# Kernel optimization log

Hardware: AMD Instinct MI355X
Metric: run time of the kernel (lower is better)

Reference implementation:

```python
import jax, jax.numpy as jnp
import numpy as np

E = 8  # moe_num_experts


def setup_inputs() -> dict:
    key = jax.random.key(0)
    ks = jax.random.split(key, 6)
    T, H, F, K = 8192, 768, 3072, 2
    x = jax.random.normal(ks[0], (T, H), dtype=jnp.float32)
    weights = jax.random.uniform(ks[1], (T, E), dtype=jnp.float32)
    top_weights = jax.random.uniform(ks[2], (T, K), dtype=jnp.float32)
    top_experts = jax.random.randint(ks[3], (T, K), 0, E)
    w1 = jax.random.normal(ks[4], (E, F, H), dtype=jnp.float32) * 0.02
    w2 = jax.random.normal(ks[5], (E, F, H), dtype=jnp.float32) * 0.02
    bias = jnp.zeros((H,), dtype=jnp.float32)
    return {"x": x, "weights": weights, "top_weights": top_weights,
            "top_experts": top_experts, "w1": w1, "w2": w2, "bias": bias}


def reference(x, weights, top_weights, top_experts, w1, w2, bias):
    # combine[t, e] = sum_k top_weights[t, k] * 1[top_experts[t, k] == e]
    one_hot = jax.nn.one_hot(top_experts, E, dtype=x.dtype)  # [T, K, E]
    combine = jnp.einsum('tke,tk->te', one_hot, top_weights)  # [T, E]
    out = jnp.zeros_like(x)
    for e in range(E):  # fixed small expert loop
        h = jax.nn.gelu(x @ w1[e].T, approximate=False)  # [T, F]
        out = out + (h @ w2[e]) * combine[:, e:e + 1]
    return out + bias
```

## Files before the change

kernel.cpp:

```cpp
#include <hip/hip_runtime.h>
#include <math.h>

#define TT   8192
#define HH   768
#define FF   3072
#define NEXP 8
#define NP   16384
#define BM   128
#define MAXT 135
#define MTP  136
#define ESTR (FF*HH)

typedef unsigned short u16;
typedef __attribute__((ext_vector_type(8))) short bf16x8;
typedef __attribute__((ext_vector_type(4))) float f32x4;

__device__ __forceinline__ u16 f2b(float f) {
  unsigned u = __float_as_uint(f);
  unsigned r = (u + 0x7FFFu + ((u >> 16) & 1u)) >> 16;
  return (u16)r;
}

__device__ __forceinline__ float gelu_exact(float v) {
  return 0.5f * v * (1.0f + erff(v * 0.70710678118654752f));
}

__device__ __forceinline__ void gll16(const void* g, void* l) {
  __builtin_amdgcn_global_load_lds(
      (const __attribute__((address_space(1))) void*)g,
      (__attribute__((address_space(3))) void*)l, 16, 0, 0);
}

__global__ __launch_bounds__(1024)
void route_all(const int* __restrict__ te, const float* __restrict__ tw,
               int* __restrict__ hdr) {
  __shared__ int cnt[NEXP], offs[NEXP], cur[NEXP];
  const int tid = threadIdx.x;
  const int lane = tid & 63, wave = tid >> 6;
  if (tid < NEXP) cnt[tid] = 0;
  __syncthreads();
  for (int base = wave * 64; base < NP; base += 1024) {
    int e = te[base + lane];
#pragma unroll
    for (int x = 0; x < NEXP; ++x) {
      unsigned long long m = __ballot(e == x);
      if (lane == 0 && m) atomicAdd(&cnt[x], __popcll(m));
    }
  }
  __syncthreads();
  if (tid == 0) {
    int run = 0, tt = 0;
#pragma unroll
    for (int x = 0; x < NEXP; ++x) {
      offs[x] = run; cur[x] = run;
      hdr[x] = cnt[x]; hdr[16 + x] = run;
      run += cnt[x];
    }
    for (int x = 0; x < NEXP; ++x) {
      int nt = (cnt[x] + BM - 1) >> 7;
      for (int i = 0; i < nt; ++i) { hdr[32 + tt] = x; hdr[192 + tt] = i * BM; ++tt; }
    }
    hdr[24] = tt;
  }
  __syncthreads();
  for (int base = wave * 64; base < NP; base += 1024) {
    int i = base + lane;
    int e = te[i];
    float w = tw[i];
    int slot = 0;
#pragma unroll
    for (int x = 0; x < NEXP; ++x) {
      unsigned long long m = __ballot(e == x);
      int nb = __popcll(m);
      int below = __popcll(m & ((1ull << lane) - 1ull));
      int b = 0;
      if (lane == 0) b = nb ? atomicAdd(&cur[x], nb) : 0;
      b = __shfl(b, 0);
      if (e == x) slot = b + below;
    }
    hdr[352 + slot] = i >> 1;
    ((float*)(hdr + 16736))[slot] = w;
    hdr[33120 + i] = slot;
  }
}

__global__ void cvt_all(const float* __restrict__ x, const float* __restrict__ w1,
                        u16* __restrict__ dst, int xn4, int totn4) {
  for (int i = blockIdx.x * 256 + threadIdx.x; i < totn4; i += gridDim.x * 256) {
    float4 v = (i < xn4) ? ((const float4*)x)[i] : ((const float4*)w1)[i - xn4];
    ushort4 o;
    o.x = f2b(v.x); o.y = f2b(v.y); o.z = f2b(v.z); o.w = f2b(v.w);
    ((ushort4*)dst)[i] = o;
  }
}

__global__ void transpose_w2(const float* __restrict__ w2, u16* __restrict__ w2t) {
  __shared__ u16 t[64][65];
  int e = blockIdx.z;
  int f0 = blockIdx.x * 64, h0 = blockIdx.y * 64;
  int tid = threadIdx.x;
  int tx = tid & 15, ty = tid >> 4;
  const float* s = w2 + (size_t)e * ESTR;
#pragma unroll
  for (int j = 0; j < 4; ++j) {
    int f = f0 + ty + 16 * j;
    float4 v = *(const float4*)&s[(size_t)f * HH + h0 + tx * 4];
    t[ty + 16 * j][tx * 4 + 0] = f2b(v.x);
    t[ty + 16 * j][tx * 4 + 1] = f2b(v.y);
    t[ty + 16 * j][tx * 4 + 2] = f2b(v.z);
    t[ty + 16 * j][tx * 4 + 3] = f2b(v.w);
  }
  __syncthreads();
  u16* d = w2t + (size_t)e * ESTR;
#pragma unroll
  for (int j = 0; j < 4; ++j) {
    int hr = ty + 16 * j;
    ushort4 o;
    o.x = t[tx * 4 + 0][hr];
    o.y = t[tx * 4 + 1][hr];
    o.z = t[tx * 4 + 2][hr];
    o.w = t[tx * 4 + 3][hr];
    *(ushort4*)&d[(size_t)(h0 + hr) * FF + f0 + tx * 4] = o;
  }
}

__global__ void bias_init(float* __restrict__ out, const float* __restrict__ bias) {
  int i = blockIdx.x * 256 + threadIdx.x;
  if (i < TT * HH / 4)
    ((float4*)out)[i] = ((const float4*)bias)[i % (HH / 4)];
}

__global__ void combine(const float* __restrict__ part, const int* __restrict__ hdr,
                        const float* __restrict__ bias, float* __restrict__ out) {
  int t = blockIdx.x;
  int c = threadIdx.x;
  const int* inv = hdr + 33120;
  const float* pw = (const float*)(hdr + 16736);
  int g0 = inv[2 * t], g1 = inv[2 * t + 1];
  float w0 = pw[g0], w1 = pw[g1];
  float4 p0 = ((const float4*)(part + (size_t)g0 * HH))[c];
  float4 p1 = ((const float4*)(part + (size_t)g1 * HH))[c];
  float4 b  = ((const float4*)bias)[c];
  float4 o;
  o.x = b.x + w0 * p0.x + w1 * p1.x;
  o.y = b.y + w0 * p0.y + w1 * p1.y;
  o.z = b.z + w0 * p0.z + w1 * p1.z;
  o.w = b.w + w0 * p0.w + w1 * p1.w;
  ((float4*)(out + (size_t)t * HH))[c] = o;
}

template <int PHASE, int NT, int G, int KS>
__global__ __launch_bounds__(256, 3)
void moe_gemm(const u16* __restrict__ Asrc, const u16* __restrict__ Bsrc,
              u16* __restrict__ Hout, float* __restrict__ Out,
              const int* __restrict__ hdr) {
  constexpr int KEXT = (PHASE == 1) ? HH : (FF / KS);
  constexpr int AST  = (PHASE == 1) ? HH : FF;
  constexpr int BST  = (PHASE == 1) ? HH : FF;
  constexpr int NK   = KEXT / 32;

  const int nwg = NT * MTP * KS;
  const int bid = blockIdx.x;
  const int l   = (bid & 7) * (nwg >> 3) + (bid >> 3);
  const int mtl = l % G;
  const int nt  = (l / G) % NT;
  const int kg  = (l / (G * NT)) % KS;
  const int sg  = l / (G * NT * KS);
  const int mt  = sg * G + mtl;
  if (mt >= hdr[24]) return;
  const int kbase = kg * KEXT;

  const int e   = hdr[32 + mt];
  const int m0  = hdr[192 + mt];
  const int cnt = hdr[e];
  const int off = hdr[16 + e];
  const int* ptok = hdr + 352;

  __shared__ u16 Al[3][4096];
  __shared__ u16 Bl[3][4096];

  const int tid  = threadIdx.x;
  const int lane = tid & 63;
  const int wave = tid >> 6;
  const int wm = wave >> 1, wn = wave & 1;
  const int lr = lane & 15;

  const int kcs = (((tid & 3) ^ ((tid >> 3) & 3)) * 8);
  const u16* aptr[2];
  const u16* bptr[2];
#pragma unroll
  for (int i = 0; i < 2; ++i) {
    int r = (tid >> 2) + 64 * i;
    if (PHASE == 1) {
      int g = off + m0 + r; g = g < NP ? g : NP - 1;
      aptr[i] = Asrc + (size_t)ptok[g] * AST + kcs;
    } else {
      int gr = off + m0 + r; gr = gr < NP ? gr : NP - 1;
      aptr[i] = Asrc + (size_t)gr * AST + kbase + kcs;
    }
    int br = nt * BM + r;
    bptr[i] = Bsrc + (size_t)e * ESTR + (size_t)br * BST + kbase + kcs;
  }

  f32x4 acc[4][4] = {};
  const int pcs = (((lane >> 4) ^ ((lane >> 1) & 3)) * 8);

#define STG(BS, T) do {                              \
    gll16(aptr[0] + (T) * 32, &Al[BS][tid * 8]);     \
    gll16(aptr[1] + (T) * 32, &Al[BS][tid * 8 + 2048]); \
    gll16(bptr[0] + (T) * 32, &Bl[BS][tid * 8]);     \
    gll16(bptr[1] + (T) * 32, &Bl[BS][tid * 8 + 2048]); \
  } while (0)

#define ITER(BC, BS, TSTG, DOST, VMN) do {                                   \
    asm volatile("s_waitcnt vmcnt(" #VMN ")" ::: "memory");                  \
    __builtin_amdgcn_sched_barrier(0);                                       \
    __builtin_amdgcn_s_barrier();                                            \
    bf16x8 af[4], bfr[4];                                                    \
    _Pragma("unroll")                                                        \
    for (int i = 0; i < 4; ++i)                                              \
      af[i] = *(const bf16x8*)&Al[BC][(wm * 64 + i * 16 + lr) * 32 + pcs];   \
    _Pragma("unroll")                                                        \
    for (int i = 0; i < 4; ++i)                                              \
      bfr[i] = *(const bf16x8*)&Bl[BC][(wn * 64 + i * 16 + lr) * 32 + pcs];  \
    if (DOST) STG(BS, TSTG);                                                 \
    asm volatile("s_waitcnt lgkmcnt(0)" ::: "memory");                       \
    __builtin_amdgcn_sched_barrier(0);                                       \
    __builtin_amdgcn_s_setprio(1);                                           \
    _Pragma("unroll")                                                        \
    for (int mi = 0; mi < 4; ++mi)                                           \
      _Pragma("unroll")                                                      \
      for (int ni = 0; ni < 4; ++ni)                                         \
        acc[mi][ni] = __builtin_amdgcn_mfma_f32_16x16x32_bf16(               \
            af[mi], bfr[ni], acc[mi][ni], 0, 0, 0);                          \
    __builtin_amdgcn_s_setprio(0);                                           \
  } while (0)

  STG(0, 0);
  STG(1, 1);

  for (int g = 0; g < NK / 3 - 1; ++g) {
    const int t0 = g * 3;
    ITER(0, 2, t0 + 2, 1, 4);
    ITER(1, 0, t0 + 3, 1, 4);
    ITER(2, 1, t0 + 4, 1, 4);
  }
  ITER(0, 2, NK - 1, 1, 4);
  ITER(1, 0, 0, 0, 4);
  ITER(2, 0, 0, 0, 0);
#undef ITER
#undef STG

  if (PHASE == 1) {
#pragma unroll
    for (int mi = 0; mi < 4; ++mi)
#pragma unroll
      for (int ni = 0; ni < 4; ++ni)
#pragma unroll
        for (int j = 0; j < 4; ++j) {
          int rl = wm * 64 + mi * 16 + (lane >> 4) * 4 + j;
          int gr = m0 + rl;
          if (gr < cnt) {
            int col = nt * BM + wn * 64 + ni * 16 + lr;
            Hout[(size_t)(off + gr) * FF + col] = f2b(gelu_exact(acc[mi][ni][j]));
          }
        }
  } else {
#pragma unroll
    for (int mi = 0; mi < 4; ++mi)
#pragma unroll
      for (int ni = 0; ni < 4; ++ni)
#pragma unroll
        for (int j = 0; j < 4; ++j) {
          int rl = wm * 64 + mi * 16 + (lane >> 4) * 4 + j;
          int gr = m0 + rl;
          if (gr < cnt) {
            int col = nt * BM + wn * 64 + ni * 16 + lr;
            Out[(size_t)(off + gr) * HH + col] = acc[mi][ni][j];
          }
        }
  }
}

__global__ void naive_pair(const float* __restrict__ x, const float* __restrict__ tw,
                           const int* __restrict__ te, const float* __restrict__ w1,
                           const float* __restrict__ w2, float* __restrict__ out) {
  __shared__ float xs[HH];
  __shared__ float hb[FF];
  int t = blockIdx.x >> 1, k = blockIdx.x & 1;
  int e = te[t * 2 + k];
  float wt = tw[t * 2 + k];
  for (int i = threadIdx.x; i < HH; i += 256) xs[i] = x[(size_t)t * HH + i];
  __syncthreads();
  const float* W1 = w1 + (size_t)e * ESTR;
  for (int f = threadIdx.x; f < FF; f += 256) {
    float s = 0.f;
    const float* r = W1 + (size_t)f * HH;
    for (int i = 0; i < HH; ++i) s += xs[i] * r[i];
    hb[f] = gelu_exact(s);
  }
  __syncthreads();
  const float* W2 = w2 + (size_t)e * ESTR;
  for (int c = threadIdx.x; c < HH; c += 256) {
    float s = 0.f;
    for (int f = 0; f < FF; ++f) s += hb[f] * W2[(size_t)f * HH + c];
    atomicAdd(&out[(size_t)t * HH + c], s * wt);
  }
}

extern "C" void kernel_launch(void* const* d_in, const int* in_sizes, int n_in,
                              void* d_out, int out_size, void* d_ws, size_t ws_size,
                              hipStream_t stream) {
  const float* x    = (const float*)d_in[0];
  const float* topw = (const float*)d_in[2];
  const int*   tope = (const int*)d_in[3];
  const float* w1   = (const float*)d_in[4];
  const float* w2   = (const float*)d_in[5];
  const float* bias = (const float*)d_in[6];
  float* out = (float*)d_out;

  char* ws = (char*)d_ws;
  const size_t HDRB   = 1u << 18;
  const size_t xb_off  = HDRB;
  const size_t xb_sz   = (size_t)TT * HH * 2;
  const size_t w1_off  = xb_off + xb_sz;
  const size_t w1_sz   = (size_t)NEXP * ESTR * 2;
  const size_t w2t_off = w1_off + w1_sz;
  const size_t w2t_sz  = w1_sz;
  const size_t h_off   = w2t_off + w2t_sz;
  const size_t h_sz    = (size_t)NP * FF * 2;
  const size_t need    = h_off + h_sz;

  if (ws_size < need) {
    bias_init<<<(TT * HH / 4 + 255) / 256, 256, 0, stream>>>(out, bias);
    naive_pair<<<NP, 256, 0, stream>>>(x, topw, tope, w1, w2, out);
    return;
  }

  int* hdr   = (int*)ws;
  u16* xb    = (u16*)(ws + xb_off);
  u16* w1b   = (u16*)(ws + w1_off);
  u16* w2t   = (u16*)(ws + w2t_off);
  u16* h     = (u16*)(ws + h_off);
  float* part = (float*)(ws + xb_off);

  route_all<<<1, 1024, 0, stream>>>(tope, topw, hdr);

  const int XN4 = TT * HH / 4;
  const int TOTN4 = (TT * HH + NEXP * ESTR) / 4;
  cvt_all<<<2048, 256, 0, stream>>>(x, w1, xb, XN4, TOTN4);
  transpose_w2<<<dim3(FF / 64, HH / 64, NEXP), 256, 0, stream>>>(w2, w2t);

  moe_gemm<1, 24, 8, 1><<<24 * MTP, 256, 0, stream>>>(xb, w1b, h, nullptr, hdr);
  moe_gemm<2, 6, 4, 1><<<6 * MTP, 256, 0, stream>>>(h, w2t, nullptr, part, hdr);
  combine<<<TT, HH / 4, 0, stream>>>(part, hdr, bias, out);
}
```

Before: 356.1 us.

## Load B operand directly to registers and deepen A LDS pipeline to four stages

The grouped MoE GEMM no longer stages the weight (B) tile through LDS. Each wave loads its B fragments straight from global memory into double-buffered registers, one k-step ahead. Only the gathered activation (A) tile still goes through LDS, now with a 4-deep ring buffer and a vmcnt(2) wait. Halving the LDS footprint lets launch_bounds rise to 4 blocks per CU, and the unused KS split-K template parameter is removed; the trade-off is uncoalesced per-lane B loads and more register pressure.

After: 720.9 us. +102.4%, slower.

```diff
diff --git a/kernel.cpp b/kernel.cpp
--- a/kernel.cpp
+++ b/kernel.cpp
@@ -34,7 +34,7 @@
 __global__ __launch_bounds__(1024)
 void route_all(const int* __restrict__ te, const float* __restrict__ tw,
                int* __restrict__ hdr) {
-  __shared__ int cnt[NEXP], offs[NEXP], cur[NEXP];
+  __shared__ int cnt[NEXP], cur[NEXP];
   const int tid = threadIdx.x;
   const int lane = tid & 63, wave = tid >> 6;
   if (tid < NEXP) cnt[tid] = 0;
@@ -52,7 +52,7 @@
     int run = 0, tt = 0;
 #pragma unroll
     for (int x = 0; x < NEXP; ++x) {
-      offs[x] = run; cur[x] = run;
+      cur[x] = run;
       hdr[x] = cnt[x]; hdr[16 + x] = run;
       run += cnt[x];
     }
@@ -149,26 +149,24 @@
   ((float4*)(out + (size_t)t * HH))[c] = o;
 }
 
-template <int PHASE, int NT, int G, int KS>
-__global__ __launch_bounds__(256, 3)
+template <int PHASE, int NT, int G>
+__global__ __launch_bounds__(256, 4)
 void moe_gemm(const u16* __restrict__ Asrc, const u16* __restrict__ Bsrc,
               u16* __restrict__ Hout, float* __restrict__ Out,
               const int* __restrict__ hdr) {
-  constexpr int KEXT = (PHASE == 1) ? HH : (FF / KS);
+  constexpr int KEXT = (PHASE == 1) ? HH : FF;
   constexpr int AST  = (PHASE == 1) ? HH : FF;
   constexpr int BST  = (PHASE == 1) ? HH : FF;
   constexpr int NK   = KEXT / 32;
 
-  const int nwg = NT * MTP * KS;
+  const int nwg = NT * MTP;
   const int bid = blockIdx.x;
   const int l   = (bid & 7) * (nwg >> 3) + (bid >> 3);
   const int mtl = l % G;
   const int nt  = (l / G) % NT;
-  const int kg  = (l / (G * NT)) % KS;
-  const int sg  = l / (G * NT * KS);
+  const int sg  = l / (G * NT);
   const int mt  = sg * G + mtl;
   if (mt >= hdr[24]) return;
-  const int kbase = kg * KEXT;
 
   const int e   = hdr[32 + mt];
   const int m0  = hdr[192 + mt];
@@ -176,8 +174,7 @@
   const int off = hdr[16 + e];
   const int* ptok = hdr + 352;
 
-  __shared__ u16 Al[3][4096];
-  __shared__ u16 Bl[3][4096];
+  __shared__ u16 Al[4][4096];
 
   const int tid  = threadIdx.x;
   const int lane = tid & 63;
@@ -187,7 +184,6 @@
 
   const int kcs = (((tid & 3) ^ ((tid >> 3) & 3)) * 8);
   const u16* aptr[2];
-  const u16* bptr[2];
 #pragma unroll
   for (int i = 0; i < 2; ++i) {
     int r = (tid >> 2) + 64 * i;
@@ -196,34 +192,43 @@
       aptr[i] = Asrc + (size_t)ptok[g] * AST + kcs;
     } else {
       int gr = off + m0 + r; gr = gr < NP ? gr : NP - 1;
-      aptr[i] = Asrc + (size_t)gr * AST + kbase + kcs;
-    }
-    int br = nt * BM + r;
-    bptr[i] = Bsrc + (size_t)e * ESTR + (size_t)br * BST + kbase + kcs;
+      aptr[i] = Asrc + (size_t)gr * AST + kcs;
+    }
+  }
+  const u16* bp[4];
+#pragma unroll
+  for (int q = 0; q < 4; ++q) {
+    int row = nt * BM + wn * 64 + q * 16 + lr;
+    bp[q] = Bsrc + (size_t)e * ESTR + (size_t)row * BST + (lane >> 4) * 8;
   }
 
   f32x4 acc[4][4] = {};
   const int pcs = (((lane >> 4) ^ ((lane >> 1) & 3)) * 8);
-
-#define STG(BS, T) do {                              \
-    gll16(aptr[0] + (T) * 32, &Al[BS][tid * 8]);     \
-    gll16(aptr[1] + (T) * 32, &Al[BS][tid * 8 + 2048]); \
-    gll16(bptr[0] + (T) * 32, &Bl[BS][tid * 8]);     \
-    gll16(bptr[1] + (T) * 32, &Bl[BS][tid * 8 + 2048]); \
+  bf16x8 brA[4], brB[4];
+
+#define STG(BS, T) do {                                   \
+    gll16(aptr[0] + (T) * 32, &Al[BS][tid * 8]);          \
+    gll16(aptr[1] + (T) * 32, &Al[BS][tid * 8 + 2048]);   \
   } while (0)
 
-#define ITER(BC, BS, TSTG, DOST, VMN) do {                                   \
+#define LDB(br, T) do {                                   \
+    _Pragma("unroll")                                     \
+    for (int q = 0; q < 4; ++q)                           \
+      br[q] = *(const bf16x8*)(bp[q] + (T) * 32);         \
+  } while (0)
+
+#define ITER(ABUF, brUSE, brLD, T, DOB, DOA, VMN) do {                       \
     asm volatile("s_waitcnt vmcnt(" #VMN ")" ::: "memory");                  \
     __builtin_amdgcn_sched_barrier(0);                                       \
     __builtin_amdgcn_s_barrier();                                            \
-    bf16x8 af[4], bfr[4];                                                    \
+    bf16x8 af[4];                                                            \
     _Pragma("unroll")                                                        \
     for (int i = 0; i < 4; ++i)                                              \
-      af[i] = *(const bf16x8*)&Al[BC][(wm * 64 + i * 16 + lr) * 32 + pcs];   \
-    _Pragma("unroll")                                                        \
-    for (int i = 0; i < 4; ++i)                                              \
-      bfr[i] = *(const bf16x8*)&Bl[BC][(wn * 64 + i * 16 + lr) * 32 + pcs];  \
-    if (DOST) STG(BS, TSTG);                                                 \
+      af[i] = *(const bf16x8*)&Al[ABUF][(wm * 64 + i * 16 + lr) * 32 + pcs]; \
+    if (DOB) LDB(brLD, (T) + 1);                                             \
+    __builtin_amdgcn_sched_barrier(0);                                       \
+    if (DOA) STG(((T) + 2) & 3, (T) + 2);                                    \
+    __builtin_amdgcn_sched_barrier(0);                                       \
     asm volatile("s_waitcnt lgkmcnt(0)" ::: "memory");                       \
     __builtin_amdgcn_sched_barrier(0);                                       \
     __builtin_amdgcn_s_setprio(1);                                           \
@@ -232,23 +237,27 @@
       _Pragma("unroll")                                                      \
       for (int ni = 0; ni < 4; ++ni)                                         \
         acc[mi][ni] = __builtin_amdgcn_mfma_f32_16x16x32_bf16(               \
-            af[mi], bfr[ni], acc[mi][ni], 0, 0, 0);                          \
+            af[mi], brUSE[ni], acc[mi][ni], 0, 0, 0);                        \
     __builtin_amdgcn_s_setprio(0);                                           \
   } while (0)
 
+  LDB(brA, 0);
+  __builtin_amdgcn_sched_barrier(0);
   STG(0, 0);
   STG(1, 1);
 
-  for (int g = 0; g < NK / 3 - 1; ++g) {
-    const int t0 = g * 3;
-    ITER(0, 2, t0 + 2, 1, 4);
-    ITER(1, 0, t0 + 3, 1, 4);
-    ITER(2, 1, t0 + 4, 1, 4);
-  }
-  ITER(0, 2, NK - 1, 1, 4);
-  ITER(1, 0, 0, 0, 4);
-  ITER(2, 0, 0, 0, 0);
+  for (int t0 = 0; t0 < NK - 4; t0 += 4) {
+    ITER(0, brA, brB, t0 + 0, 1, 1, 2);
+    ITER(1, brB, brA, t0 + 1, 1, 1, 2);
+    ITER(2, brA, brB, t0 + 2, 1, 1, 2);
+    ITER(3, brB, brA, t0 + 3, 1, 1, 2);
+  }
+  ITER(0, brA, brB, NK - 4, 1, 1, 2);
+  ITER(1, brB, brA, NK - 3, 1, 1, 2);
+  ITER(2, brA, brB, NK - 2, 1, 0, 2);
+  ITER(3, brB, brA, NK - 1, 0, 0, 0);
 #undef ITER
+#undef LDB
 #undef STG
 
   if (PHASE == 1) {
@@ -351,7 +360,7 @@
   cvt_all<<<2048, 256, 0, stream>>>(x, w1, xb, XN4, TOTN4);
   transpose_w2<<<dim3(FF / 64, HH / 64, NEXP), 256, 0, stream>>>(w2, w2t);
 
-  moe_gemm<1, 24, 8, 1><<<24 * MTP, 256, 0, stream>>>(xb, w1b, h, nullptr, hdr);
-  moe_gemm<2, 6, 4, 1><<<6 * MTP, 256, 0, stream>>>(h, w2t, nullptr, part, hdr);
+  moe_gemm<1, 24, 8><<<24 * MTP, 256, 0, stream>>>(xb, w1b, h, nullptr, hdr);
+  moe_gemm<2, 6, 4><<<6 * MTP, 256, 0, stream>>>(h, w2t, nullptr, part, hdr);
   combine<<<TT, HH / 4, 0, stream>>>(part, hdr, bias, out);
 }
```

## Use 256-row M tiles with 512-thread blocks for the first expert GEMM

Applied to the files above, without the earlier changes.

Splits the shared expert GEMM into two kernels. The first GEMM (x·w1 with GELU) now uses 256-row token tiles, 8 waves and 512 threads per block, so each loaded w1 tile feeds twice as many rows. This halves w1 reloads and the number of workgroups. The router builds a second tile list for the 256-row tiles in a new header region, and the second GEMM keeps its 128-row configuration. The cost is more padding waste in each expert's last tile, more LDS per block, and tighter register and occupancy limits from the 512-thread launch bounds.

Measured after the change: 350.7 us. Within noise of the previous version (-1.5%).

```diff
diff --git a/kernel.cpp b/kernel.cpp
--- a/kernel.cpp
+++ b/kernel.cpp
@@ -7,8 +7,9 @@
 #define NEXP 8
 #define NP   16384
 #define BM   128
-#define MAXT 135
+#define BM1  256
 #define MTP  136
+#define MTP1 72
 #define ESTR (FF*HH)
 
 typedef unsigned short u16;
@@ -34,7 +35,7 @@
 __global__ __launch_bounds__(1024)
 void route_all(const int* __restrict__ te, const float* __restrict__ tw,
                int* __restrict__ hdr) {
-  __shared__ int cnt[NEXP], offs[NEXP], cur[NEXP];
+  __shared__ int cnt[NEXP], cur[NEXP];
   const int tid = threadIdx.x;
   const int lane = tid & 63, wave = tid >> 6;
   if (tid < NEXP) cnt[tid] = 0;
@@ -49,18 +50,20 @@
   }
   __syncthreads();
   if (tid == 0) {
-    int run = 0, tt = 0;
+    int run = 0, t1 = 0, t2 = 0;
 #pragma unroll
     for (int x = 0; x < NEXP; ++x) {
-      offs[x] = run; cur[x] = run;
+      cur[x] = run;
       hdr[x] = cnt[x]; hdr[16 + x] = run;
       run += cnt[x];
     }
     for (int x = 0; x < NEXP; ++x) {
-      int nt = (cnt[x] + BM - 1) >> 7;
-      for (int i = 0; i < nt; ++i) { hdr[32 + tt] = x; hdr[192 + tt] = i * BM; ++tt; }
+      int n1 = (cnt[x] + BM - 1) >> 7;
+      for (int i = 0; i < n1; ++i) { hdr[32 + t1] = x; hdr[192 + t1] = i * BM; ++t1; }
+      int n2 = (cnt[x] + BM1 - 1) >> 8;
+      for (int i = 0; i < n2; ++i) { hdr[49504 + t2] = x; hdr[49576 + t2] = i * BM1; ++t2; }
     }
-    hdr[24] = tt;
+    hdr[8] = t1; hdr[9] = t2;
   }
   __syncthreads();
   for (int base = wave * 64; base < NP; base += 1024) {
@@ -149,34 +152,27 @@
   ((float4*)(out + (size_t)t * HH))[c] = o;
 }
 
-template <int PHASE, int NT, int G, int KS>
-__global__ __launch_bounds__(256, 3)
-void moe_gemm(const u16* __restrict__ Asrc, const u16* __restrict__ Bsrc,
-              u16* __restrict__ Hout, float* __restrict__ Out,
-              const int* __restrict__ hdr) {
-  constexpr int KEXT = (PHASE == 1) ? HH : (FF / KS);
-  constexpr int AST  = (PHASE == 1) ? HH : FF;
-  constexpr int BST  = (PHASE == 1) ? HH : FF;
-  constexpr int NK   = KEXT / 32;
-
-  const int nwg = NT * MTP * KS;
+template <int NT, int G>
+__global__ __launch_bounds__(512, 4)
+void moe_gemm1(const u16* __restrict__ Asrc, const u16* __restrict__ Bsrc,
+               u16* __restrict__ Hout, const int* __restrict__ hdr) {
+  constexpr int NK = HH / 32;
+  const int nwg = NT * MTP1;
   const int bid = blockIdx.x;
   const int l   = (bid & 7) * (nwg >> 3) + (bid >> 3);
   const int mtl = l % G;
   const int nt  = (l / G) % NT;
-  const int kg  = (l / (G * NT)) % KS;
-  const int sg  = l / (G * NT * KS);
+  const int sg  = l / (G * NT);
   const int mt  = sg * G + mtl;
-  if (mt >= hdr[24]) return;
-  const int kbase = kg * KEXT;
-
-  const int e   = hdr[32 + mt];
-  const int m0  = hdr[192 + mt];
+  if (mt >= hdr[9]) return;
+
+  const int e   = hdr[49504 + mt];
+  const int m0  = hdr[49576 + mt];
   const int cnt = hdr[e];
   const int off = hdr[16 + e];
   const int* ptok = hdr + 352;
 
-  __shared__ u16 Al[3][4096];
+  __shared__ u16 Al[3][8192];
   __shared__ u16 Bl[3][4096];
 
   const int tid  = threadIdx.x;
@@ -187,29 +183,22 @@
 
   const int kcs = (((tid & 3) ^ ((tid >> 3) & 3)) * 8);
   const u16* aptr[2];
-  const u16* bptr[2];
 #pragma unroll
   for (int i = 0; i < 2; ++i) {
-    int r = (tid >> 2) + 64 * i;
-    if (PHASE == 1) {
-      int g = off + m0 + r; g = g < NP ? g : NP - 1;
-      aptr[i] = Asrc + (size_t)ptok[g] * AST + kcs;
-    } else {
-      int gr = off + m0 + r; gr = gr < NP ? gr : NP - 1;
-      aptr[i] = Asrc + (size_t)gr * AST + kbase + kcs;
-    }
-    int br = nt * BM + r;
-    bptr[i] = Bsrc + (size_t)e * ESTR + (size_t)br * BST + kbase + kcs;
-  }
+    int r = (tid >> 2) + 128 * i;
+    int g = off + m0 + r; g = g < NP ? g : NP - 1;
+    aptr[i] = Asrc + (size_t)ptok[g] * HH + kcs;
+  }
+  const u16* bptr = Bsrc + (size_t)e * ESTR +
+                    (size_t)(nt * BM + (tid >> 2)) * HH + kcs;
 
   f32x4 acc[4][4] = {};
   const int pcs = (((lane >> 4) ^ ((lane >> 1) & 3)) * 8);
 
-#define STG(BS, T) do {                              \
-    gll16(aptr[0] + (T) * 32, &Al[BS][tid * 8]);     \
-    gll16(aptr[1] + (T) * 32, &Al[BS][tid * 8 + 2048]); \
-    gll16(bptr[0] + (T) * 32, &Bl[BS][tid * 8]);     \
-    gll16(bptr[1] + (T) * 32, &Bl[BS][tid * 8 + 2048]); \
+#define STG(BS, T) do {                                   \
+    gll16(aptr[0] + (T) * 32, &Al[BS][tid * 8]);          \
+    gll16(aptr[1] + (T) * 32, &Al[BS][tid * 8 + 4096]);   \
+    gll16(bptr + (T) * 32, &Bl[BS][tid * 8]);             \
   } while (0)
 
 #define ITER(BC, BS, TSTG, DOST, VMN) do {                                   \
@@ -241,6 +230,110 @@
 
   for (int g = 0; g < NK / 3 - 1; ++g) {
     const int t0 = g * 3;
+    ITER(0, 2, t0 + 2, 1, 3);
+    ITER(1, 0, t0 + 3, 1, 3);
+    ITER(2, 1, t0 + 4, 1, 3);
+  }
+  ITER(0, 2, NK - 1, 1, 3);
+  ITER(1, 0, 0, 0, 3);
+  ITER(2, 0, 0, 0, 0);
+#undef ITER
+#undef STG
+
+#pragma unroll
+  for (int mi = 0; mi < 4; ++mi)
+#pragma unroll
+    for (int ni = 0; ni < 4; ++ni)
+#pragma unroll
+      for (int j = 0; j < 4; ++j) {
+        int rl = wm * 64 + mi * 16 + (lane >> 4) * 4 + j;
+        int gr = m0 + rl;
+        if (gr < cnt) {
+          int col = nt * BM + wn * 64 + ni * 16 + lr;
+          Hout[(size_t)(off + gr) * FF + col] = f2b(gelu_exact(acc[mi][ni][j]));
+        }
+      }
+}
+
+template <int NT, int G>
+__global__ __launch_bounds__(256, 3)
+void moe_gemm2(const u16* __restrict__ Asrc, const u16* __restrict__ Bsrc,
+               float* __restrict__ Out, const int* __restrict__ hdr) {
+  constexpr int NK = FF / 32;
+  const int nwg = NT * MTP;
+  const int bid = blockIdx.x;
+  const int l   = (bid & 7) * (nwg >> 3) + (bid >> 3);
+  const int mtl = l % G;
+  const int nt  = (l / G) % NT;
+  const int sg  = l / (G * NT);
+  const int mt  = sg * G + mtl;
+  if (mt >= hdr[8]) return;
+
+  const int e   = hdr[32 + mt];
+  const int m0  = hdr[192 + mt];
+  const int cnt = hdr[e];
+  const int off = hdr[16 + e];
+
+  __shared__ u16 Al[3][4096];
+  __shared__ u16 Bl[3][4096];
+
+  const int tid  = threadIdx.x;
+  const int lane = tid & 63;
+  const int wave = tid >> 6;
+  const int wm = wave >> 1, wn = wave & 1;
+  const int lr = lane & 15;
+
+  const int kcs = (((tid & 3) ^ ((tid >> 3) & 3)) * 8);
+  const u16* aptr[2];
+  const u16* bptr[2];
+#pragma unroll
+  for (int i = 0; i < 2; ++i) {
+    int r = (tid >> 2) + 64 * i;
+    int gr = off + m0 + r; gr = gr < NP ? gr : NP - 1;
+    aptr[i] = Asrc + (size_t)gr * FF + kcs;
+    int br = nt * BM + r;
+    bptr[i] = Bsrc + (size_t)e * ESTR + (size_t)br * FF + kcs;
+  }
+
+  f32x4 acc[4][4] = {};
+  const int pcs = (((lane >> 4) ^ ((lane >> 1) & 3)) * 8);
+
+#define STG(BS, T) do {                                 \
+    gll16(aptr[0] + (T) * 32, &Al[BS][tid * 8]);        \
+    gll16(aptr[1] + (T) * 32, &Al[BS][tid * 8 + 2048]); \
+    gll16(bptr[0] + (T) * 32, &Bl[BS][tid * 8]);        \
+    gll16(bptr[1] + (T) * 32, &Bl[BS][tid * 8 + 2048]); \
+  } while (0)
+
+#define ITER(BC, BS, TSTG, DOST, VMN) do {                                   \
+    asm volatile("s_waitcnt vmcnt(" #VMN ")" ::: "memory");                  \
+    __builtin_amdgcn_sched_barrier(0);                                       \
+    __builtin_amdgcn_s_barrier();                                            \
+    bf16x8 af[4], bfr[4];                                                    \
+    _Pragma("unroll")                                                        \
+    for (int i = 0; i < 4; ++i)                                              \
+      af[i] = *(const bf16x8*)&Al[BC][(wm * 64 + i * 16 + lr) * 32 + pcs];   \
+    _Pragma("unroll")                                                        \
+    for (int i = 0; i < 4; ++i)                                              \
+      bfr[i] = *(const bf16x8*)&Bl[BC][(wn * 64 + i * 16 + lr) * 32 + pcs];  \
+    if (DOST) STG(BS, TSTG);                                                 \
+    asm volatile("s_waitcnt lgkmcnt(0)" ::: "memory");                       \
+    __builtin_amdgcn_sched_barrier(0);                                       \
+    __builtin_amdgcn_s_setprio(1);                                           \
+    _Pragma("unroll")                                                        \
+    for (int mi = 0; mi < 4; ++mi)                                           \
+      _Pragma("unroll")                                                      \
+      for (int ni = 0; ni < 4; ++ni)                                         \
+        acc[mi][ni] = __builtin_amdgcn_mfma_f32_16x16x32_bf16(               \
+            af[mi], bfr[ni], acc[mi][ni], 0, 0, 0);                          \
+    __builtin_amdgcn_s_setprio(0);                                           \
+  } while (0)
+
+  STG(0, 0);
+  STG(1, 1);
+
+  for (int g = 0; g < NK / 3 - 1; ++g) {
+    const int t0 = g * 3;
     ITER(0, 2, t0 + 2, 1, 4);
     ITER(1, 0, t0 + 3, 1, 4);
     ITER(2, 1, t0 + 4, 1, 4);
@@ -251,35 +344,19 @@
 #undef ITER
 #undef STG
 
-  if (PHASE == 1) {
-#pragma unroll
-    for (int mi = 0; mi < 4; ++mi)
-#pragma unroll
-      for (int ni = 0; ni < 4; ++ni)
-#pragma unroll
-        for (int j = 0; j < 4; ++j) {
-          int rl = wm * 64 + mi * 16 + (lane >> 4) * 4 + j;
-          int gr = m0 + rl;
-          if (gr < cnt) {
-            int col = nt * BM + wn * 64 + ni * 16 + lr;
-            Hout[(size_t)(off + gr) * FF + col] = f2b(gelu_exact(acc[mi][ni][j]));
-          }
+#pragma unroll
+  for (int mi = 0; mi < 4; ++mi)
+#pragma unroll
+    for (int ni = 0; ni < 4; ++ni)
+#pragma unroll
+      for (int j = 0; j < 4; ++j) {
+        int rl = wm * 64 + mi * 16 + (lane >> 4) * 4 + j;
+        int gr = m0 + rl;
+        if (gr < cnt) {
+          int col = nt * BM + wn * 64 + ni * 16 + lr;
+          Out[(size_t)(off + gr) * HH + col] = acc[mi][ni][j];
         }
-  } else {
-#pragma unroll
-    for (int mi = 0; mi < 4; ++mi)
-#pragma unroll
-      for (int ni = 0; ni < 4; ++ni)
-#pragma unroll
-        for (int j = 0; j < 4; ++j) {
-          int rl = wm * 64 + mi * 16 + (lane >> 4) * 4 + j;
-          int gr = m0 + rl;
-          if (gr < cnt) {
-            int col = nt * BM + wn * 64 + ni * 16 + lr;
-            Out[(size_t)(off + gr) * HH + col] = acc[mi][ni][j];
-          }
-        }
-  }
+      }
 }
 
 __global__ void naive_pair(const float* __restrict__ x, const float* __restrict__ tw,
@@ -351,7 +428,7 @@
   cvt_all<<<2048, 256, 0, stream>>>(x, w1, xb, XN4, TOTN4);
   transpose_w2<<<dim3(FF / 64, HH / 64, NEXP), 256, 0, stream>>>(w2, w2t);
 
-  moe_gemm<1, 24, 8, 1><<<24 * MTP, 256, 0, stream>>>(xb, w1b, h, nullptr, hdr);
-  moe_gemm<2, 6, 4, 1><<<6 * MTP, 256, 0, stream>>>(h, w2t, nullptr, part, hdr);
+  moe_gemm1<24, 8><<<24 * MTP1, 512, 0, stream>>>(xb, w1b, h, hdr);
+  moe_gemm2<6, 4><<<6 * MTP, 256, 0, stream>>>(h, w2t, part, hdr);
   combine<<<TT, HH / 4, 0, stream>>>(part, hdr, bias, out);
 }
```

## Enlarge GEMM M-tile to 256 with 512-thread blocks and bf16 partial outputs

Applied to the files above, without the earlier changes.

Both grouped GEMM phases now use 256-row M tiles run by 8 waves per 512-thread block, sharing one 128-row B tile per K step. This halves the weight-tile loads per output and cuts the number of workgroups. The routing header gets a new tile table for the 256-row tiles. The phase-2 partial results are stored as bf16 instead of fp32, which halves write and read traffic into the combine kernel but adds rounding error. More LDS per block and fewer, larger tiles may lower occupancy and leave more padding waste in each expert's last tile.

Measured after the change: 322.1 us. 9.5% less time.

```diff
diff --git a/kernel.cpp b/kernel.cpp
--- a/kernel.cpp
+++ b/kernel.cpp
@@ -7,8 +7,8 @@
 #define NEXP 8
 #define NP   16384
 #define BM   128
-#define MAXT 135
-#define MTP  136
+#define BM1  256
+#define MTP1 72
 #define ESTR (FF*HH)
 
 typedef unsigned short u16;
@@ -21,6 +21,10 @@
   return (u16)r;
 }
 
+__device__ __forceinline__ float b2f(u16 b) {
+  return __uint_as_float(((unsigned)b) << 16);
+}
+
 __device__ __forceinline__ float gelu_exact(float v) {
   return 0.5f * v * (1.0f + erff(v * 0.70710678118654752f));
 }
@@ -34,7 +38,7 @@
 __global__ __launch_bounds__(1024)
 void route_all(const int* __restrict__ te, const float* __restrict__ tw,
                int* __restrict__ hdr) {
-  __shared__ int cnt[NEXP], offs[NEXP], cur[NEXP];
+  __shared__ int cnt[NEXP], cur[NEXP];
   const int tid = threadIdx.x;
   const int lane = tid & 63, wave = tid >> 6;
   if (tid < NEXP) cnt[tid] = 0;
@@ -49,18 +53,18 @@
   }
   __syncthreads();
   if (tid == 0) {
-    int run = 0, tt = 0;
+    int run = 0, t2 = 0;
 #pragma unroll
     for (int x = 0; x < NEXP; ++x) {
-      offs[x] = run; cur[x] = run;
+      cur[x] = run;
       hdr[x] = cnt[x]; hdr[16 + x] = run;
       run += cnt[x];
     }
     for (int x = 0; x < NEXP; ++x) {
-      int nt = (cnt[x] + BM - 1) >> 7;
-      for (int i = 0; i < nt; ++i) { hdr[32 + tt] = x; hdr[192 + tt] = i * BM; ++tt; }
+      int n2 = (cnt[x] + BM1 - 1) >> 8;
+      for (int i = 0; i < n2; ++i) { hdr[49504 + t2] = x; hdr[49576 + t2] = i * BM1; ++t2; }
     }
-    hdr[24] = tt;
+    hdr[9] = t2;
   }
   __syncthreads();
   for (int base = wave * 64; base < NP; base += 1024) {
@@ -130,7 +134,7 @@
     ((float4*)out)[i] = ((const float4*)bias)[i % (HH / 4)];
 }
 
-__global__ void combine(const float* __restrict__ part, const int* __restrict__ hdr,
+__global__ void combine(const u16* __restrict__ part, const int* __restrict__ hdr,
                         const float* __restrict__ bias, float* __restrict__ out) {
   int t = blockIdx.x;
   int c = threadIdx.x;
@@ -138,45 +142,43 @@
   const float* pw = (const float*)(hdr + 16736);
   int g0 = inv[2 * t], g1 = inv[2 * t + 1];
   float w0 = pw[g0], w1 = pw[g1];
-  float4 p0 = ((const float4*)(part + (size_t)g0 * HH))[c];
-  float4 p1 = ((const float4*)(part + (size_t)g1 * HH))[c];
+  ushort4 p0 = ((const ushort4*)(part + (size_t)g0 * HH))[c];
+  ushort4 p1 = ((const ushort4*)(part + (size_t)g1 * HH))[c];
   float4 b  = ((const float4*)bias)[c];
   float4 o;
-  o.x = b.x + w0 * p0.x + w1 * p1.x;
-  o.y = b.y + w0 * p0.y + w1 * p1.y;
-  o.z = b.z + w0 * p0.z + w1 * p1.z;
-  o.w = b.w + w0 * p0.w + w1 * p1.w;
+  o.x = b.x + w0 * b2f(p0.x) + w1 * b2f(p1.x);
+  o.y = b.y + w0 * b2f(p0.y) + w1 * b2f(p1.y);
+  o.z = b.z + w0 * b2f(p0.z) + w1 * b2f(p1.z);
+  o.w = b.w + w0 * b2f(p0.w) + w1 * b2f(p1.w);
   ((float4*)(out + (size_t)t * HH))[c] = o;
 }
 
-template <int PHASE, int NT, int G, int KS>
-__global__ __launch_bounds__(256, 3)
+template <int PHASE, int NT, int G>
+__global__ __launch_bounds__(512, 4)
 void moe_gemm(const u16* __restrict__ Asrc, const u16* __restrict__ Bsrc,
-              u16* __restrict__ Hout, float* __restrict__ Out,
-              const int* __restrict__ hdr) {
-  constexpr int KEXT = (PHASE == 1) ? HH : (FF / KS);
+              u16* __restrict__ Outp, const int* __restrict__ hdr) {
+  constexpr int KEXT = (PHASE == 1) ? HH : FF;
   constexpr int AST  = (PHASE == 1) ? HH : FF;
   constexpr int BST  = (PHASE == 1) ? HH : FF;
+  constexpr int OST  = (PHASE == 1) ? FF : HH;
   constexpr int NK   = KEXT / 32;
 
-  const int nwg = NT * MTP * KS;
+  const int nwg = NT * MTP1;
   const int bid = blockIdx.x;
   const int l   = (bid & 7) * (nwg >> 3) + (bid >> 3);
   const int mtl = l % G;
   const int nt  = (l / G) % NT;
-  const int kg  = (l / (G * NT)) % KS;
-  const int sg  = l / (G * NT * KS);
+  const int sg  = l / (G * NT);
   const int mt  = sg * G + mtl;
-  if (mt >= hdr[24]) return;
-  const int kbase = kg * KEXT;
-
-  const int e   = hdr[32 + mt];
-  const int m0  = hdr[192 + mt];
+  if (mt >= hdr[9]) return;
+
+  const int e   = hdr[49504 + mt];
+  const int m0  = hdr[49576 + mt];
   const int cnt = hdr[e];
   const int off = hdr[16 + e];
   const int* ptok = hdr + 352;
 
-  __shared__ u16 Al[3][4096];
+  __shared__ u16 Al[3][8192];
   __shared__ u16 Bl[3][4096];
 
   const int tid  = threadIdx.x;
@@ -187,29 +189,25 @@
 
   const int kcs = (((tid & 3) ^ ((tid >> 3) & 3)) * 8);
   const u16* aptr[2];
-  const u16* bptr[2];
 #pragma unroll
   for (int i = 0; i < 2; ++i) {
-    int r = (tid >> 2) + 64 * i;
-    if (PHASE == 1) {
-      int g = off + m0 + r; g = g < NP ? g : NP - 1;
+    int r = (tid >> 2) + 128 * i;
+    int g = off + m0 + r; g = g < NP ? g : NP - 1;
+    if (PHASE == 1)
       aptr[i] = Asrc + (size_t)ptok[g] * AST + kcs;
-    } else {
-      int gr = off + m0 + r; gr = gr < NP ? gr : NP - 1;
-      aptr[i] = Asrc + (size_t)gr * AST + kbase + kcs;
-    }
-    int br = nt * BM + r;
-    bptr[i] = Bsrc + (size_t)e * ESTR + (size_t)br * BST + kbase + kcs;
-  }
+    else
+      aptr[i] = Asrc + (size_t)g * AST + kcs;
+  }
+  const u16* bptr = Bsrc + (size_t)e * ESTR +
+                    (size_t)(nt * BM + (tid >> 2)) * BST + kcs;
 
   f32x4 acc[4][4] = {};
   const int pcs = (((lane >> 4) ^ ((lane >> 1) & 3)) * 8);
 
-#define STG(BS, T) do {                              \
-    gll16(aptr[0] + (T) * 32, &Al[BS][tid * 8]);     \
-    gll16(aptr[1] + (T) * 32, &Al[BS][tid * 8 + 2048]); \
-    gll16(bptr[0] + (T) * 32, &Bl[BS][tid * 8]);     \
-    gll16(bptr[1] + (T) * 32, &Bl[BS][tid * 8 + 2048]); \
+#define STG(BS, T) do {                                   \
+    gll16(aptr[0] + (T) * 32, &Al[BS][tid * 8]);          \
+    gll16(aptr[1] + (T) * 32, &Al[BS][tid * 8 + 4096]);   \
+    gll16(bptr + (T) * 32, &Bl[BS][tid * 8]);             \
   } while (0)
 
 #define ITER(BC, BS, TSTG, DOST, VMN) do {                                   \
@@ -241,45 +239,31 @@
 
   for (int g = 0; g < NK / 3 - 1; ++g) {
     const int t0 = g * 3;
-    ITER(0, 2, t0 + 2, 1, 4);
-    ITER(1, 0, t0 + 3, 1, 4);
-    ITER(2, 1, t0 + 4, 1, 4);
-  }
-  ITER(0, 2, NK - 1, 1, 4);
-  ITER(1, 0, 0, 0, 4);
+    ITER(0, 2, t0 + 2, 1, 3);
+    ITER(1, 0, t0 + 3, 1, 3);
+    ITER(2, 1, t0 + 4, 1, 3);
+  }
+  ITER(0, 2, NK - 1, 1, 3);
+  ITER(1, 0, 0, 0, 3);
   ITER(2, 0, 0, 0, 0);
 #undef ITER
 #undef STG
 
-  if (PHASE == 1) {
-#pragma unroll
-    for (int mi = 0; mi < 4; ++mi)
-#pragma unroll
-      for (int ni = 0; ni < 4; ++ni)
-#pragma unroll
-        for (int j = 0; j < 4; ++j) {
-          int rl = wm * 64 + mi * 16 + (lane >> 4) * 4 + j;
-          int gr = m0 + rl;
-          if (gr < cnt) {
-            int col = nt * BM + wn * 64 + ni * 16 + lr;
-            Hout[(size_t)(off + gr) * FF + col] = f2b(gelu_exact(acc[mi][ni][j]));
-          }
+#pragma unroll
+  for (int mi = 0; mi < 4; ++mi)
+#pragma unroll
+    for (int ni = 0; ni < 4; ++ni)
+#pragma unroll
+      for (int j = 0; j < 4; ++j) {
+        int rl = wm * 64 + mi * 16 + (lane >> 4) * 4 + j;
+        int gr = m0 + rl;
+        if (gr < cnt) {
+          int col = nt * BM + wn * 64 + ni * 16 + lr;
+          float v = acc[mi][ni][j];
+          if (PHASE == 1) v = gelu_exact(v);
+          Outp[(size_t)(off + gr) * OST + col] = f2b(v);
         }
-  } else {
-#pragma unroll
-    for (int mi = 0; mi < 4; ++mi)
-#pragma unroll
-      for (int ni = 0; ni < 4; ++ni)
-#pragma unroll
-        for (int j = 0; j < 4; ++j) {
-          int rl = wm * 64 + mi * 16 + (lane >> 4) * 4 + j;
-          int gr = m0 + rl;
-          if (gr < cnt) {
-            int col = nt * BM + wn * 64 + ni * 16 + lr;
-            Out[(size_t)(off + gr) * HH + col] = acc[mi][ni][j];
-          }
-        }
-  }
+      }
 }
 
 __global__ void naive_pair(const float* __restrict__ x, const float* __restrict__ tw,
@@ -342,7 +326,7 @@
   u16* w1b   = (u16*)(ws + w1_off);
   u16* w2t   = (u16*)(ws + w2t_off);
   u16* h     = (u16*)(ws + h_off);
-  float* part = (float*)(ws + xb_off);
+  u16* part  = (u16*)(ws + xb_off);
 
   route_all<<<1, 1024, 0, stream>>>(tope, topw, hdr);
 
@@ -351,7 +335,7 @@
   cvt_all<<<2048, 256, 0, stream>>>(x, w1, xb, XN4, TOTN4);
   transpose_w2<<<dim3(FF / 64, HH / 64, NEXP), 256, 0, stream>>>(w2, w2t);
 
-  moe_gemm<1, 24, 8, 1><<<24 * MTP, 256, 0, stream>>>(xb, w1b, h, nullptr, hdr);
-  moe_gemm<2, 6, 4, 1><<<6 * MTP, 256, 0, stream>>>(h, w2t, nullptr, part, hdr);
+  moe_gemm<1, 24, 8><<<24 * MTP1, 512, 0, stream>>>(xb, w1b, h, hdr);
+  moe_gemm<2, 6, 2><<<6 * MTP1, 512, 0, stream>>>(h, w2t, part, hdr);
   combine<<<TT, HH / 4, 0, stream>>>(part, hdr, bias, out);
 }
```
